# Optimization experiments

Measured on AMD Instinct MI355X. Metric: run time of the kernel, lower is better.

The kernel has to match this reference:

```python
import jax, jax.numpy as jnp
import numpy as np

# DAG configuration (fixed, mirrors the networkx dG used at construction time)
B = 4096          # batch
N_INP = 4096      # genes
L0 = 512          # leaf GO terms, each mapped to G disjoint genes
G = 8             # genes per leaf term
H = 16            # module_neurons (uniform per-module hidden size)
FAN = 8           # children per internal module -> input size FAN*H = 128
L1, L2 = 64, 8    # internal level sizes; root has L2=8 children


def setup_inputs() -> dict:
    key = jax.random.key(0)
    ks = jax.random.split(key, 8)
    s = lambda *sh: 0.1
    x = jax.random.normal(ks[0], (B, N_INP), dtype=jnp.float32)
    # Gene (RestrictedLayer) effective weights: kernel*connections is one-hot,
    # so only kernel[gene_idx[m,j], j] survives -> store as [L0, G] + bias.
    Wg = jax.random.normal(ks[1], (L0, G), dtype=jnp.float32) * 0.1
    bg = jax.random.normal(ks[2], (L0, G), dtype=jnp.float32) * 0.1
    # Per-level module Dense kernels (sigmoid, no bias)
    W0 = jax.random.normal(ks[3], (L0, G, H), dtype=jnp.float32) * 0.1       # leaf terms: G -> H
    W1 = jax.random.normal(ks[4], (L1, FAN * H, H), dtype=jnp.float32) * 0.1  # 128 -> 16
    W2 = jax.random.normal(ks[5], (L2, FAN * H, H), dtype=jnp.float32) * 0.1  # 128 -> 16
    W3 = jax.random.normal(ks[6], (FAN * H, H), dtype=jnp.float32) * 0.1      # root: 128 -> 16
    Wf = jax.random.normal(ks[7], (H, 1), dtype=jnp.float32) * 0.1            # final linear, no bias
    return {"x": x, "Wg": Wg, "bg": bg, "W0": W0, "W1": W1, "W2": W2,
            "W3": W3, "Wf": Wf}


def reference(x, Wg, bg, W0, W1, W2, W3, Wf):
    b = x.shape[0]
    # Input gene layers (RestrictedLayer, linear activation):
    # leaf m owns contiguous genes [m*G, (m+1)*G) -> gather is a reshape.
    gene_out = x.reshape(b, L0, G) * Wg + bg                    # [B, L0, G]
    # Level 0 (leaf GO terms): Dense(G->H), sigmoid, no bias
    h0 = jax.nn.sigmoid(jnp.einsum('bmg,mgh->bmh', gene_out, W0))   # [B, L0, H]
    # Level 1: concat FAN children's H outputs -> Dense(FAN*H -> H), sigmoid
    h1 = jax.nn.sigmoid(jnp.einsum('bmk,mkh->bmh',
                                   h0.reshape(b, L1, FAN * H), W1))  # [B, L1, H]
    # Level 2
    h2 = jax.nn.sigmoid(jnp.einsum('bmk,mkh->bmh',
                                   h1.reshape(b, L2, FAN * H), W2))  # [B, L2, H]
    # Root 'GO:output'
    hr = jax.nn.sigmoid(h2.reshape(b, FAN * H) @ W3)                 # [B, H]
    # Final Dense(1), linear, no bias
    return hr @ Wf                                                   # [B, 1]
```

## Files before the change

### kernel.cpp

```cpp
#include <hip/hip_runtime.h>
#include <hip/hip_bf16.h>


#define TB 8
#define H0S 1032
#define H1S 136

typedef __attribute__((ext_vector_type(8))) short short8;
typedef __attribute__((ext_vector_type(4))) float floatx4;

__device__ __forceinline__ float sigf(float v) {
    return __builtin_amdgcn_rcpf(1.0f + __expf(-v));
}
__device__ __forceinline__ unsigned int f2bf_u32(float f) {
    unsigned int u = __builtin_bit_cast(unsigned int, f);
    return (u + 0x7fffu + ((u >> 16) & 1u)) >> 16;
}
__device__ __forceinline__ unsigned short f2bf(float f) {
    return (unsigned short)f2bf_u32(f);
}
__device__ __forceinline__ unsigned int f2bf2(float lo, float hi) {
    return f2bf_u32(lo) | (f2bf_u32(hi) << 16);
}

__global__ __launch_bounds__(256) void k_prep(
    const float* __restrict__ W1, const float* __restrict__ W2,
    unsigned short* __restrict__ W1t, unsigned short* __restrict__ W2t)
{
    __shared__ float wl[128 * 17];
    const int mb = blockIdx.x;
    const float* src = (mb < 64) ? (W1 + (size_t)mb * 2048)
                                 : (W2 + (size_t)(mb - 64) * 2048);
    unsigned short* dst = (mb < 64) ? (W1t + (size_t)mb * 2048)
                                    : (W2t + (size_t)(mb - 64) * 2048);
    const int tid = threadIdx.x;
#pragma unroll
    for (int i = 0; i < 8; ++i) {
        const int idx = tid + i * 256;
        wl[(idx >> 4) * 17 + (idx & 15)] = src[idx];
    }
    __syncthreads();
#pragma unroll
    for (int i = 0; i < 4; ++i) {
        const int u  = tid + i * 256;
        const int h  = u >> 6;
        const int k  = (u & 63) * 2;
        ((unsigned int*)dst)[u] = f2bf2(wl[k * 17 + h], wl[(k + 1) * 17 + h]);
    }
}

__global__ __launch_bounds__(256) void k_tree(
    const float* __restrict__ x, const float* __restrict__ Wg,
    const float* __restrict__ bg, const float* __restrict__ W0,
    const unsigned short* __restrict__ W1t, const unsigned short* __restrict__ W2t,
    float* __restrict__ h2ws)
{
    __shared__ __align__(16) unsigned short h0s[TB * H0S];
    __shared__ __align__(16) unsigned short h1s[TB * H1S];

    const int tid  = threadIdx.x;
    const int s    = blockIdx.x & 7;
    const int b0   = (blockIdx.x >> 3) * TB;
    const int lane = tid & 63;
    const int wv   = tid >> 6;
    const int m_l  = tid >> 2;
    const int hq   = tid & 3;
    const int m    = s * 64 + m_l;

    float4 w0r[8];
#pragma unroll
    for (int g = 0; g < 8; ++g)
        w0r[g] = *(const float4*)(W0 + (size_t)m * 128 + g * 16 + hq * 4);
    const float4 wg0 = *(const float4*)(Wg + m * 8);
    const float4 wg1 = *(const float4*)(Wg + m * 8 + 4);
    const float4 bg0 = *(const float4*)(bg + m * 8);
    const float4 bg1 = *(const float4*)(bg + m * 8 + 4);

    {
        const float* xb = x + (size_t)b0 * 4096 + s * 512 + m_l * 8;
        unsigned short* h0base = &h0s[m_l * 16 + hq * 4];
#pragma unroll
        for (int b = 0; b < TB; ++b) {
            const float4 xv0 = *(const float4*)(xb + (size_t)b * 4096);
            const float4 xv1 = *(const float4*)(xb + (size_t)b * 4096 + 4);
            float gene[8];
            gene[0] = fmaf(xv0.x, wg0.x, bg0.x);
            gene[1] = fmaf(xv0.y, wg0.y, bg0.y);
            gene[2] = fmaf(xv0.z, wg0.z, bg0.z);
            gene[3] = fmaf(xv0.w, wg0.w, bg0.w);
            gene[4] = fmaf(xv1.x, wg1.x, bg1.x);
            gene[5] = fmaf(xv1.y, wg1.y, bg1.y);
            gene[6] = fmaf(xv1.z, wg1.z, bg1.z);
            gene[7] = fmaf(xv1.w, wg1.w, bg1.w);
            float a0 = 0.f, a1 = 0.f, a2 = 0.f, a3 = 0.f;
#pragma unroll
            for (int g = 0; g < 8; ++g) {
                a0 = fmaf(gene[g], w0r[g].x, a0);
                a1 = fmaf(gene[g], w0r[g].y, a1);
                a2 = fmaf(gene[g], w0r[g].z, a2);
                a3 = fmaf(gene[g], w0r[g].w, a3);
            }
            *(uint2*)(h0base + b * H0S) =
                make_uint2(f2bf2(sigf(a0), sigf(a1)), f2bf2(sigf(a2), sigf(a3)));
        }
    }
    __syncthreads();

    const int n = lane & 15, q = lane >> 4;
    {
#pragma unroll
        for (int jj = 0; jj < 2; ++jj) {
            const int j = wv * 2 + jj;
            const unsigned short* w1m =
                W1t + ((size_t)(s * 8 + j) * 16 + n) * 128 + q * 8;
            const unsigned short* am = &h0s[(n & 7) * H0S + j * 128 + q * 8];
            floatx4 acc = {0.f, 0.f, 0.f, 0.f};
#pragma unroll
            for (int ks = 0; ks < 4; ++ks) {
                const short8 av = *(const short8*)(am + ks * 32);
                const short8 bv = *(const short8*)(w1m + ks * 32);
                acc = __builtin_amdgcn_mfma_f32_16x16x32_bf16(av, bv, acc, 0, 0, 0);
            }
            if (q < 2) {
#pragma unroll
                for (int r = 0; r < 4; ++r)
                    h1s[(q * 4 + r) * H1S + j * 16 + n] = f2bf(sigf(acc[r]));
            }
        }
    }
    __syncthreads();

    if (wv == 0) {
        const unsigned short* w2m = W2t + ((size_t)s * 16 + n) * 128 + q * 8;
        const unsigned short* am = &h1s[(n & 7) * H1S + q * 8];
        floatx4 acc = {0.f, 0.f, 0.f, 0.f};
#pragma unroll
        for (int ks = 0; ks < 4; ++ks) {
            const short8 av = *(const short8*)(am + ks * 32);
            const short8 bv = *(const short8*)(w2m + ks * 32);
            acc = __builtin_amdgcn_mfma_f32_16x16x32_bf16(av, bv, acc, 0, 0, 0);
        }
        if (q < 2) {
#pragma unroll
            for (int r = 0; r < 4; ++r)
                h2ws[(size_t)(b0 + q * 4 + r) * 128 + s * 16 + n] = sigf(acc[r]);
        }
    }
}

__global__ __launch_bounds__(128) void k_root(
    const float* __restrict__ h2ws, const float* __restrict__ W3,
    const float* __restrict__ Wf, float* __restrict__ out)
{
    __shared__ float w3s[2048];
    __shared__ float wfs[16];
    const int tid = threadIdx.x;
#pragma unroll
    for (int t = 0; t < 16; ++t) w3s[tid + t * 128] = W3[tid + t * 128];
    if (tid < 16) wfs[tid] = Wf[tid];
    __syncthreads();

    const int h = tid & 15;
    const int b = blockIdx.x * 8 + (tid >> 4);
    const float4* hp = (const float4*)(h2ws + (size_t)b * 128);
    float acc = 0.f;
#pragma unroll
    for (int k4 = 0; k4 < 32; ++k4) {
        const float4 hv = hp[k4];
        acc = fmaf(hv.x, w3s[(k4 * 4 + 0) * 16 + h], acc);
        acc = fmaf(hv.y, w3s[(k4 * 4 + 1) * 16 + h], acc);
        acc = fmaf(hv.z, w3s[(k4 * 4 + 2) * 16 + h], acc);
        acc = fmaf(hv.w, w3s[(k4 * 4 + 3) * 16 + h], acc);
    }
    float v = sigf(acc) * wfs[h];
    v += __shfl_down(v, 8, 16);
    v += __shfl_down(v, 4, 16);
    v += __shfl_down(v, 2, 16);
    v += __shfl_down(v, 1, 16);
    if (h == 0) out[b] = v;
}

extern "C" void kernel_launch(void* const* d_in, const int* in_sizes, int n_in,
                              void* d_out, int out_size, void* d_ws, size_t ws_size,
                              hipStream_t stream) {
    const float* x  = (const float*)d_in[0];
    const float* Wg = (const float*)d_in[1];
    const float* bg = (const float*)d_in[2];
    const float* W0 = (const float*)d_in[3];
    const float* W1 = (const float*)d_in[4];
    const float* W2 = (const float*)d_in[5];
    const float* W3 = (const float*)d_in[6];
    const float* Wf = (const float*)d_in[7];
    float* out = (float*)d_out;

    float* h2 = (float*)d_ws;
    unsigned short* W1t = (unsigned short*)((char*)d_ws + (size_t)2 * 1024 * 1024);
    unsigned short* W2t = W1t + (size_t)64 * 2048;

    k_prep<<<dim3(72), dim3(256), 0, stream>>>(W1, W2, W1t, W2t);
    k_tree<<<dim3((4096 / TB) * 8), dim3(256), 0, stream>>>(x, Wg, bg, W0, W1t, W2t, h2);
    k_root<<<dim3(4096 / 8), dim3(128), 0, stream>>>(h2, W3, Wf, out);
}
```

Before: 129.9 us.

## Move leaf layer onto MFMA with folded gene weights and 16-row batch tiles

The gene scaling and leaf Dense layer are folded algebraically into a prepacked bf16 block-diagonal weight (Wg*W0 scaled by -log2e) plus a precomputed bias. The leaf layer then runs on 16x16x32 bf16 MFMA, with x converted to bf16, and sigmoid computed through exp2. The batch tile grows from 8 to 16 rows so the level-1 and level-2 MFMAs use all 16 M rows instead of wasting half, which halves the grid. In exchange, x is rounded to bf16 and the sparse padded leaf MFMAs do extra wasted work.

```diff
diff --git a/kernel.cpp b/kernel.cpp
--- a/kernel.cpp
+++ b/kernel.cpp
@@ -2,12 +2,13 @@
 #include <hip/hip_bf16.h>
 
 
-#define TB 8
 #define H0S 1032
 #define H1S 136
+#define C2N (-1.4426950408889634f)
 
 typedef __attribute__((ext_vector_type(8))) short short8;
 typedef __attribute__((ext_vector_type(4))) float floatx4;
+typedef __attribute__((ext_vector_type(4))) unsigned int uint4v;
 
 __device__ __forceinline__ float sigf(float v) {
     return __builtin_amdgcn_rcpf(1.0f + __expf(-v));
@@ -25,95 +26,117 @@
 
 __global__ __launch_bounds__(256) void k_prep(
     const float* __restrict__ W1, const float* __restrict__ W2,
-    unsigned short* __restrict__ W1t, unsigned short* __restrict__ W2t)
+    const float* __restrict__ W0, const float* __restrict__ Wg,
+    const float* __restrict__ bg,
+    unsigned short* __restrict__ W1t, unsigned short* __restrict__ W2t,
+    unsigned int* __restrict__ W0z, float* __restrict__ cbias)
 {
     __shared__ float wl[128 * 17];
     const int mb = blockIdx.x;
-    const float* src = (mb < 64) ? (W1 + (size_t)mb * 2048)
-                                 : (W2 + (size_t)(mb - 64) * 2048);
-    unsigned short* dst = (mb < 64) ? (W1t + (size_t)mb * 2048)
-                                    : (W2t + (size_t)(mb - 64) * 2048);
     const int tid = threadIdx.x;
-#pragma unroll
-    for (int i = 0; i < 8; ++i) {
-        const int idx = tid + i * 256;
-        wl[(idx >> 4) * 17 + (idx & 15)] = src[idx];
-    }
-    __syncthreads();
-#pragma unroll
-    for (int i = 0; i < 4; ++i) {
-        const int u  = tid + i * 256;
-        const int h  = u >> 6;
-        const int k  = (u & 63) * 2;
-        ((unsigned int*)dst)[u] = f2bf2(wl[k * 17 + h], wl[(k + 1) * 17 + h]);
+    if (mb < 72) {
+        const float* src = (mb < 64) ? (W1 + (size_t)mb * 2048)
+                                     : (W2 + (size_t)(mb - 64) * 2048);
+        unsigned short* dst = (mb < 64) ? (W1t + (size_t)mb * 2048)
+                                        : (W2t + (size_t)(mb - 64) * 2048);
+#pragma unroll
+        for (int i = 0; i < 8; ++i) {
+            const int idx = tid + i * 256;
+            wl[(idx >> 4) * 17 + (idx & 15)] = src[idx];
+        }
+        __syncthreads();
+#pragma unroll
+        for (int i = 0; i < 4; ++i) {
+            const int u = tid + i * 256;
+            const int h = u >> 6;
+            const int k = (u & 63) * 2;
+            ((unsigned int*)dst)[u] = f2bf2(wl[k * 17 + h], wl[(k + 1) * 17 + h]);
+        }
+    } else {
+        const int mb2 = mb - 72;
+#pragma unroll
+        for (int t = 0; t < 16; ++t) {
+            const int idx  = tid + t * 256;
+            const int mloc = idx >> 8;
+            const int rem  = idx & 255;
+            const int l    = rem >> 2;
+            const int j2   = rem & 3;
+            const int m    = mb2 * 16 + mloc;
+            const int n    = l & 15;
+            const int q    = l >> 4;
+            unsigned int v = 0u;
+            if (q == (m & 3)) {
+                const int g0 = 2 * j2;
+                const float f0 = C2N * Wg[m * 8 + g0]     * W0[(size_t)m * 128 + g0 * 16 + n];
+                const float f1 = C2N * Wg[m * 8 + g0 + 1] * W0[(size_t)m * 128 + (g0 + 1) * 16 + n];
+                v = f2bf2(f0, f1);
+            }
+            W0z[(size_t)m * 256 + rem] = v;
+        }
+        const int m = mb2 * 16 + (tid >> 4);
+        const int n = tid & 15;
+        float acc = 0.f;
+#pragma unroll
+        for (int g = 0; g < 8; ++g)
+            acc = fmaf(bg[m * 8 + g], W0[(size_t)m * 128 + g * 16 + n], acc);
+        cbias[m * 16 + n] = C2N * acc;
     }
 }
 
 __global__ __launch_bounds__(256) void k_tree(
-    const float* __restrict__ x, const float* __restrict__ Wg,
-    const float* __restrict__ bg, const float* __restrict__ W0,
+    const float* __restrict__ x, const unsigned int* __restrict__ W0z,
+    const float* __restrict__ cbias,
     const unsigned short* __restrict__ W1t, const unsigned short* __restrict__ W2t,
     float* __restrict__ h2ws)
 {
-    __shared__ __align__(16) unsigned short h0s[TB * H0S];
-    __shared__ __align__(16) unsigned short h1s[TB * H1S];
+    __shared__ __align__(16) unsigned short h0s[16 * H0S];
+    __shared__ __align__(16) unsigned short h1s[16 * H1S];
 
     const int tid  = threadIdx.x;
     const int s    = blockIdx.x & 7;
-    const int b0   = (blockIdx.x >> 3) * TB;
+    const int b0   = (blockIdx.x >> 3) * 16;
     const int lane = tid & 63;
     const int wv   = tid >> 6;
-    const int m_l  = tid >> 2;
-    const int hq   = tid & 3;
-    const int m    = s * 64 + m_l;
-
-    float4 w0r[8];
-#pragma unroll
-    for (int g = 0; g < 8; ++g)
-        w0r[g] = *(const float4*)(W0 + (size_t)m * 128 + g * 16 + hq * 4);
-    const float4 wg0 = *(const float4*)(Wg + m * 8);
-    const float4 wg1 = *(const float4*)(Wg + m * 8 + 4);
-    const float4 bg0 = *(const float4*)(bg + m * 8);
-    const float4 bg1 = *(const float4*)(bg + m * 8 + 4);
+    const int n    = lane & 15;
+    const int q    = lane >> 4;
 
     {
-        const float* xb = x + (size_t)b0 * 4096 + s * 512 + m_l * 8;
-        unsigned short* h0base = &h0s[m_l * 16 + hq * 4];
-#pragma unroll
-        for (int b = 0; b < TB; ++b) {
-            const float4 xv0 = *(const float4*)(xb + (size_t)b * 4096);
-            const float4 xv1 = *(const float4*)(xb + (size_t)b * 4096 + 4);
-            float gene[8];
-            gene[0] = fmaf(xv0.x, wg0.x, bg0.x);
-            gene[1] = fmaf(xv0.y, wg0.y, bg0.y);
-            gene[2] = fmaf(xv0.z, wg0.z, bg0.z);
-            gene[3] = fmaf(xv0.w, wg0.w, bg0.w);
-            gene[4] = fmaf(xv1.x, wg1.x, bg1.x);
-            gene[5] = fmaf(xv1.y, wg1.y, bg1.y);
-            gene[6] = fmaf(xv1.z, wg1.z, bg1.z);
-            gene[7] = fmaf(xv1.w, wg1.w, bg1.w);
-            float a0 = 0.f, a1 = 0.f, a2 = 0.f, a3 = 0.f;
-#pragma unroll
-            for (int g = 0; g < 8; ++g) {
-                a0 = fmaf(gene[g], w0r[g].x, a0);
-                a1 = fmaf(gene[g], w0r[g].y, a1);
-                a2 = fmaf(gene[g], w0r[g].z, a2);
-                a3 = fmaf(gene[g], w0r[g].w, a3);
+        const float* xrow = x + (size_t)(b0 + n) * 4096 + s * 512 + q * 8;
+#pragma unroll
+        for (int gi = 0; gi < 4; ++gi) {
+            const int mg = wv * 4 + gi;
+            const float* xg = xrow + mg * 32;
+            const float4 xa = *(const float4*)xg;
+            const float4 xb = *(const float4*)(xg + 4);
+            const uint4v up = {f2bf2(xa.x, xa.y), f2bf2(xa.z, xa.w),
+                               f2bf2(xb.x, xb.y), f2bf2(xb.z, xb.w)};
+            const short8 af = __builtin_bit_cast(short8, up);
+#pragma unroll
+            for (int pi = 0; pi < 4; ++pi) {
+                const int m_l = mg * 4 + pi;
+                const int m   = s * 64 + m_l;
+                const short8 bz = *(const short8*)(W0z + (size_t)m * 256 + lane * 4);
+                const float cb = cbias[m * 16 + n];
+                floatx4 acc = {0.f, 0.f, 0.f, 0.f};
+                acc = __builtin_amdgcn_mfma_f32_16x16x32_bf16(af, bz, acc, 0, 0, 0);
+#pragma unroll
+                for (int r = 0; r < 4; ++r) {
+                    const float e = __builtin_amdgcn_exp2f(acc[r] + cb);
+                    h0s[(q * 4 + r) * H0S + m_l * 16 + n] =
+                        f2bf(__builtin_amdgcn_rcpf(1.0f + e));
+                }
             }
-            *(uint2*)(h0base + b * H0S) =
-                make_uint2(f2bf2(sigf(a0), sigf(a1)), f2bf2(sigf(a2), sigf(a3)));
         }
     }
     __syncthreads();
 
-    const int n = lane & 15, q = lane >> 4;
     {
 #pragma unroll
         for (int jj = 0; jj < 2; ++jj) {
             const int j = wv * 2 + jj;
             const unsigned short* w1m =
                 W1t + ((size_t)(s * 8 + j) * 16 + n) * 128 + q * 8;
-            const unsigned short* am = &h0s[(n & 7) * H0S + j * 128 + q * 8];
+            const unsigned short* am = &h0s[n * H0S + j * 128 + q * 8];
             floatx4 acc = {0.f, 0.f, 0.f, 0.f};
 #pragma unroll
             for (int ks = 0; ks < 4; ++ks) {
@@ -121,18 +144,16 @@
                 const short8 bv = *(const short8*)(w1m + ks * 32);
                 acc = __builtin_amdgcn_mfma_f32_16x16x32_bf16(av, bv, acc, 0, 0, 0);
             }
-            if (q < 2) {
-#pragma unroll
-                for (int r = 0; r < 4; ++r)
-                    h1s[(q * 4 + r) * H1S + j * 16 + n] = f2bf(sigf(acc[r]));
-            }
+#pragma unroll
+            for (int r = 0; r < 4; ++r)
+                h1s[(q * 4 + r) * H1S + j * 16 + n] = f2bf(sigf(acc[r]));
         }
     }
     __syncthreads();
 
     if (wv == 0) {
         const unsigned short* w2m = W2t + ((size_t)s * 16 + n) * 128 + q * 8;
-        const unsigned short* am = &h1s[(n & 7) * H1S + q * 8];
+        const unsigned short* am = &h1s[n * H1S + q * 8];
         floatx4 acc = {0.f, 0.f, 0.f, 0.f};
 #pragma unroll
         for (int ks = 0; ks < 4; ++ks) {
@@ -140,11 +161,9 @@
             const short8 bv = *(const short8*)(w2m + ks * 32);
             acc = __builtin_amdgcn_mfma_f32_16x16x32_bf16(av, bv, acc, 0, 0, 0);
         }
-        if (q < 2) {
-#pragma unroll
-            for (int r = 0; r < 4; ++r)
-                h2ws[(size_t)(b0 + q * 4 + r) * 128 + s * 16 + n] = sigf(acc[r]);
-        }
+#pragma unroll
+        for (int r = 0; r < 4; ++r)
+            h2ws[(size_t)(b0 + q * 4 + r) * 128 + s * 16 + n] = sigf(acc[r]);
     }
 }
 
@@ -193,11 +212,15 @@
     const float* Wf = (const float*)d_in[7];
     float* out = (float*)d_out;
 
-    float* h2 = (float*)d_ws;
-    unsigned short* W1t = (unsigned short*)((char*)d_ws + (size_t)2 * 1024 * 1024);
-    unsigned short* W2t = W1t + (size_t)64 * 2048;
-
-    k_prep<<<dim3(72), dim3(256), 0, stream>>>(W1, W2, W1t, W2t);
-    k_tree<<<dim3((4096 / TB) * 8), dim3(256), 0, stream>>>(x, Wg, bg, W0, W1t, W2t, h2);
+    char* ws = (char*)d_ws;
+    float* h2            = (float*)ws;
+    unsigned short* W1t  = (unsigned short*)(ws + (2u << 20));
+    unsigned short* W2t  = (unsigned short*)(ws + (2u << 20) + (256u << 10));
+    unsigned int*   W0z  = (unsigned int*)(ws + (3u << 20));
+    float*          cbias = (float*)(ws + (3u << 20) + (512u << 10));
+
+    k_prep<<<dim3(104), dim3(256), 0, stream>>>(W1, W2, W0, Wg, bg,
+                                                W1t, W2t, W0z, cbias);
+    k_tree<<<dim3(2048), dim3(256), 0, stream>>>(x, W0z, cbias, W1t, W2t, h2);
     k_root<<<dim3(4096 / 8), dim3(128), 0, stream>>>(h2, W3, Wf, out);
 }
```

New measurement: 123.8 us. 4.7% less time.
